# Optimization experiments

Measured on AMD Instinct MI355X. Metric: run time of the kernel, lower is better.

Reference implementation:

```python
import jax, jax.numpy as jnp
import numpy as np

B, LC, LA = 512, 128, 16
VOCAB, E, H, POL = 100000, 300, 300, 3


def _lstm_dir(x, W_ih, W_hh, b):
    # x: [B,T,E] -> h: [B,T,H]; PyTorch gate order i,f,g,o
    xg = jnp.einsum('bte,ge->btg', x, W_ih) + b  # [B,T,4H]
    h0 = jnp.zeros((x.shape[0], W_hh.shape[1]), x.dtype)

    def step(carry, xt):
        h, c = carry
        g = xt + h @ W_hh.T
        i, f, gg, o = jnp.split(g, 4, axis=-1)
        c = jax.nn.sigmoid(f) * c + jax.nn.sigmoid(i) * jnp.tanh(gg)
        h = jax.nn.sigmoid(o) * jnp.tanh(c)
        return (h, c), h

    _, hs = jax.lax.scan(step, (h0, h0), jnp.swapaxes(xg, 0, 1))
    return jnp.swapaxes(hs, 0, 1)


def _bilstm(x, lengths, Wif, Whf, bf, Wib, Whb, bb):
    # DynamicLSTM semantics: valid positions only, zero-padded outputs.
    T = x.shape[1]
    t = jnp.arange(T)
    mask = t[None, :] < lengths[:, None]
    h_f = _lstm_dir(x, Wif, Whf, bf)
    # reverse each sequence within its valid length for the backward direction
    ridx = jnp.where(mask, lengths[:, None] - 1 - t[None, :], t[None, :])
    x_rev = jnp.take_along_axis(x, ridx[:, :, None], axis=1)
    h_b = jnp.take_along_axis(_lstm_dir(x_rev, Wib, Whb, bb), ridx[:, :, None], axis=1)
    out = jnp.concatenate([h_f, h_b], axis=-1)
    return out * mask[:, :, None].astype(out.dtype)


def _mgan(text_raw, aspect, text_left, embed, cWif, cWhf, cbf, cWib, cWhb, cbb,
          aWif, aWhf, abf, aWib, aWhb, abb, w_u, w_a2c, w_c2a, dW, db):
    ctx_len = jnp.sum(text_raw != 0, axis=1)
    asp_len = jnp.sum(aspect != 0, axis=1)
    left_len = jnp.sum(text_left != 0, axis=1)
    start, end = left_len, left_len + asp_len - 1
    ctx = embed[text_raw]  # [B,LC,E]
    asp = embed[aspect]    # [B,LA,E]
    ctx_out = _bilstm(ctx, ctx_len, cWif, cWhf, cbf, cWib, cWhb, cbb)  # [B,LC,2H]
    asp_out = _bilstm(asp, asp_len, aWif, aWhf, abf, aWib, aWhb, abb)  # [B,LA,2H]
    # LocationEncoding (vectorized weight_matrix)
    T = text_raw.shape[1]
    j = jnp.arange(T)[None, :]
    sl = (T - asp_len)[:, None].astype(ctx_out.dtype)
    s, e = start[:, None], end[:, None]
    w = jnp.where(j < s, 1.0 - (s - j) / sl,
                  jnp.where(j <= e, 0.0, 1.0 - (j - e) / sl)).astype(ctx_out.dtype)
    ctx_out = ctx_out * w[:, :, None]
    ctx_pool = jnp.sum(ctx_out, axis=1) / ctx_len[:, None].astype(ctx_out.dtype)  # [B,2H]
    asp_pool = jnp.sum(asp_out, axis=1) / asp_len[:, None].astype(asp_out.dtype)  # [B,2H]
    # AlignmentMatrix as one batched bilinear: w_u = [w1; w2; w3]
    w1, w2, w3 = jnp.split(w_u[:, 0], 3)
    align = (ctx_out @ w1)[:, :, None] + (asp_out @ w2)[:, None, :] \
        + jnp.einsum('bid,bjd,d->bij', ctx_out, asp_out, w3)  # [B,LC,LA]
    f_asp2ctx = jnp.einsum('bid,bi->bd', ctx_out, jax.nn.softmax(align.max(axis=2), axis=1))
    f_ctx2asp = jnp.einsum('bjd,bj->bd', asp_out, jax.nn.softmax(align.max(axis=1), axis=1))
    a1 = jax.nn.softmax(jnp.einsum('bid,de,be->bi', ctx_out, w_a2c, asp_pool), axis=1)
    c_asp2ctx = jnp.einsum('bid,bi->bd', ctx_out, a1)
    a2 = jax.nn.softmax(jnp.einsum('bjd,de,be->bj', asp_out, w_c2a, ctx_pool), axis=1)
    c_ctx2asp = jnp.einsum('bjd,bj->bd', asp_out, a2)
    feat = jnp.concatenate([c_asp2ctx, f_asp2ctx, f_ctx2asp, c_ctx2asp], axis=1)  # [B,8H]
    return feat @ dW.T + db


def setup_inputs() -> dict:
    rng = np.random.RandomState(0)
    left = rng.randint(5, 61, size=B)
    alen = rng.randint(2, LA + 1, size=B)
    right = rng.randint(5, 46, size=B)
    clen = left + alen + right  # <= 121 <= LC
    text_raw = np.zeros((B, LC), np.int64)
    aspect = np.zeros((B, LA), np.int64)
    text_left = np.zeros((B, LC), np.int64)
    for i in range(B):
        text_raw[i, :clen[i]] = rng.randint(1, VOCAB, size=clen[i])
        aspect[i, :alen[i]] = rng.randint(1, VOCAB, size=alen[i])
        text_left[i, :left[i]] = rng.randint(1, VOCAB, size=left[i])
    ks = jax.random.split(jax.random.key(0), 18)
    kk = 1.0 / np.sqrt(H)
    u = lambda k_, sh: jax.random.uniform(k_, sh, jnp.float32, -kk, kk)
    return {
        'text_raw_indices': jnp.asarray(text_raw),
        'aspect_indices': jnp.asarray(aspect),
        'text_left_indices': jnp.asarray(text_left),
        'embed': jax.random.normal(ks[0], (VOCAB, E), jnp.float32) * 0.1,
        'cWif': u(ks[1], (4 * H, E)), 'cWhf': u(ks[2], (4 * H, H)), 'cbf': u(ks[3], (4 * H,)),
        'cWib': u(ks[4], (4 * H, E)), 'cWhb': u(ks[5], (4 * H, H)), 'cbb': u(ks[6], (4 * H,)),
        'aWif': u(ks[7], (4 * H, E)), 'aWhf': u(ks[8], (4 * H, H)), 'abf': u(ks[9], (4 * H,)),
        'aWib': u(ks[10], (4 * H, E)), 'aWhb': u(ks[11], (4 * H, H)), 'abb': u(ks[12], (4 * H,)),
        'w_u': jax.random.normal(ks[13], (6 * H, 1), jnp.float32) * 0.05,
        'w_a2c': jax.random.normal(ks[14], (2 * H, 2 * H), jnp.float32) * 0.05,
        'w_c2a': jax.random.normal(ks[15], (2 * H, 2 * H), jnp.float32) * 0.05,
        'dW': u(ks[16], (POL, 8 * H)), 'db': u(ks[17], (POL,)),
    }


def reference(text_raw_indices, aspect_indices, text_left_indices, embed,
              cWif, cWhf, cbf, cWib, cWhb, cbb,
              aWif, aWhf, abf, aWib, aWhb, abb,
              w_u, w_a2c, w_c2a, dW, db):
    return _mgan(text_raw_indices, aspect_indices, text_left_indices, embed,
                 cWif, cWhf, cbf, cWib, cWhb, cbb,
                 aWif, aWhf, abf, aWib, aWhb, abb,
                 w_u, w_a2c, w_c2a, dW, db)
```

## Files before the change

kernel.cpp:

```cpp
#include <hip/hip_runtime.h>
#include <math.h>

#define BB 512
#define LC 128
#define LA 16
#define EE 300
#define HH 300
#define D2 600

__device__ __forceinline__ float sigf(float x){ return 1.0f/(1.0f+expf(-x)); }

__global__ void k_lengths(const int* __restrict__ traw, const int* __restrict__ tasp,
                          const int* __restrict__ tleft,
                          int* __restrict__ clen, int* __restrict__ alen, int* __restrict__ sstart){
  int b = blockIdx.x*blockDim.x + threadIdx.x;
  if (b >= BB) return;
  int c=0,a=0,l=0;
  for (int t=0;t<LC;t++) c += (traw[b*LC+t]!=0);
  for (int t=0;t<LA;t++) a += (tasp[b*LA+t]!=0);
  for (int t=0;t<LC;t++) l += (tleft[b*LC+t]!=0);
  clen[b]=c; alen[b]=a; sstart[b]=l;
}

__global__ void k_prep(const float* __restrict__ cWif,const float* __restrict__ cWhf,
                       const float* __restrict__ cWib,const float* __restrict__ cWhb,
                       const float* __restrict__ aWif,const float* __restrict__ aWhf,
                       const float* __restrict__ aWib,const float* __restrict__ aWhb,
                       float* __restrict__ WT4){
  const int m = blockIdx.z;
  const float* src;
  switch(m){
    case 0: src=cWif; break; case 1: src=cWhf; break;
    case 2: src=cWib; break; case 3: src=cWhb; break;
    case 4: src=aWif; break; case 5: src=aWhf; break;
    case 6: src=aWib; break; default: src=aWhb; break;
  }
  int rem = blockIdx.x*blockDim.x + threadIdx.x;
  if (rem >= 90000) return;
  int kq = rem/1200, n = rem - kq*1200;
  float4 v = *(const float4*)(src + (size_t)n*300 + kq*4);
  ((float4*)WT4)[(size_t)m*90000 + rem] = v;
}

__device__ __forceinline__ void kloop8(const float (*__restrict__ src)[300],
                                       const float* __restrict__ W,
                                       float* a0, float* a1, float* a2,
                                       int n0, int n1, int n2, bool has3){
  const float4* Wp = (const float4*)W;
  for (int kq=0; kq<75; ++kq){
    float4 w0 = Wp[n0];
    float4 w1 = Wp[n1];
    #pragma unroll
    for (int r=0;r<8;r++){
      float4 h4 = *(const float4*)&src[r][4*kq];
      a0[r]=fmaf(w0.w,h4.w,fmaf(w0.z,h4.z,fmaf(w0.y,h4.y,fmaf(w0.x,h4.x,a0[r]))));
      a1[r]=fmaf(w1.w,h4.w,fmaf(w1.z,h4.z,fmaf(w1.y,h4.y,fmaf(w1.x,h4.x,a1[r]))));
    }
    if (has3){
      float4 w2 = Wp[n2];
      #pragma unroll
      for (int r=0;r<8;r++){
        float4 h4 = *(const float4*)&src[r][4*kq];
        a2[r]=fmaf(w2.w,h4.w,fmaf(w2.z,h4.z,fmaf(w2.y,h4.y,fmaf(w2.x,h4.x,a2[r]))));
      }
    }
    Wp += 1200;
  }
}

__launch_bounds__(512,1)
__global__ void k_xg(const int* __restrict__ traw, const float* __restrict__ embed,
                     const float* __restrict__ WT4,
                     const float* __restrict__ cbf, const float* __restrict__ cbb,
                     const int* __restrict__ clen,
                     float* __restrict__ xgcf, float* __restrict__ xgcb){
  const int bid = blockIdx.x;
  const int dir = bid & 1;
  const int blkInJob = bid >> 1;
  const float* Wi = WT4 + (size_t)(dir?2:0)*360000;
  const float* bias = dir ? cbb : cbf;
  float* xg = dir ? xgcb : xgcf;
  const int tid = threadIdx.x;
  const int n0=tid, n1=tid+512, n2=tid+1024;
  const bool has3 = tid<176;

  __shared__ __align__(16) float emb16[16][300];
  __shared__ int tk[16];

  const float b0 = bias[n0], b1 = bias[n1], b2 = has3 ? bias[n2] : 0.f;

  for (int tile = blkInJob; tile < 4096; tile += 256){
    const int b = tile >> 3;
    const int t0 = (tile & 7)*16;
    const int len = clen[b];
    if (t0 >= len) continue;
    const int cnt = min(16, len - t0);
    if (tid < 16){
      int t = t0 + tid;
      int pos = dir ? (len-1-t) : t;
      tk[tid] = (tid < cnt) ? traw[b*LC + pos] : 0;
    }
    __syncthreads();
    for (int idx=tid; idx<cnt*300; idx+=512){
      int r = idx/300, e = idx - r*300;
      emb16[r][e] = embed[(size_t)tk[r]*EE + e];
    }
    __syncthreads();

    float a0[16], a1[16], a2[16];
    #pragma unroll
    for (int r=0;r<16;r++){ a0[r]=b0; a1[r]=b1; a2[r]=b2; }
    {
      const float4* Wp = (const float4*)Wi;
      for (int kq=0; kq<75; ++kq){
        float4 w0 = Wp[n0];
        float4 w1 = Wp[n1];
        #pragma unroll
        for (int r=0;r<16;r++){
          float4 h4 = *(const float4*)&emb16[r][4*kq];
          a0[r]=fmaf(w0.w,h4.w,fmaf(w0.z,h4.z,fmaf(w0.y,h4.y,fmaf(w0.x,h4.x,a0[r]))));
          a1[r]=fmaf(w1.w,h4.w,fmaf(w1.z,h4.z,fmaf(w1.y,h4.y,fmaf(w1.x,h4.x,a1[r]))));
        }
        if (has3){
          float4 w2 = Wp[n2];
          #pragma unroll
          for (int r=0;r<16;r++){
            float4 h4 = *(const float4*)&emb16[r][4*kq];
            a2[r]=fmaf(w2.w,h4.w,fmaf(w2.z,h4.z,fmaf(w2.y,h4.y,fmaf(w2.x,h4.x,a2[r]))));
          }
        }
        Wp += 1200;
      }
    }
    #pragma unroll
    for (int r=0;r<16;r++){
      if (r < cnt){
        size_t base = ((size_t)b*LC + t0 + r)*1200;
        xg[base+n0]=a0[r]; xg[base+n1]=a1[r];
        if (has3) xg[base+n2]=a2[r];
      }
    }
    __syncthreads();
  }
}

__launch_bounds__(512,1)
__global__ void k_rec(const int* __restrict__ traw, const int* __restrict__ tasp,
                      const float* __restrict__ embed,
                      const float* __restrict__ WT4,
                      const float* __restrict__ cbf, const float* __restrict__ cbb,
                      const float* __restrict__ abf, const float* __restrict__ abb,
                      const float* __restrict__ xgcf, const float* __restrict__ xgcb,
                      const int* __restrict__ clen, const int* __restrict__ alen,
                      const int* __restrict__ sstart,
                      float* __restrict__ ctx_out, float* __restrict__ asp_out, int use_xg)
{
  const int tid = threadIdx.x;
  const int job = blockIdx.x & 3;
  const int sub = blockIdx.x >> 2;
  const int row0 = sub*8;
  const int isCtx = (job < 2), bwd = (job & 1);
  const int T = isCtx ? LC : LA;
  const int* lenp = isCtx ? clen : alen;
  const int* tokp = isCtx ? traw : tasp;
  const float* Wi = WT4 + (size_t)(job*2)*360000;
  const float* Wh = Wi + 360000;
  const float* bias = (job==0)?cbf:(job==1)?cbb:(job==2)?abf:abb;
  float* outb = isCtx ? ctx_out : asp_out;
  const int coloff = bwd ? 300 : 0;
  const int fuseX = isCtx ? (!use_xg) : 1;
  const float* xg = bwd ? xgcb : xgcf;

  __shared__ __align__(16) float hb[2][8][300];
  __shared__ __align__(16) float xb[8][300];
  __shared__ float gs[8][1200];
  __shared__ int  tok_s[8][LC];
  __shared__ int  len_s[8];
  __shared__ float wins[8], wine[8], winl[8];

  if (fuseX){
    for (int idx=tid; idx<8*T; idx+=512){ int r=idx/T, t=idx-r*T; tok_s[r][t]=tokp[(row0+r)*T+t]; }
  }
  if (tid < 8){
    int b = row0 + tid; len_s[tid] = lenp[b];
    if (isCtx){ float s=(float)sstart[b], a=(float)alen[b];
      wins[tid]=s; wine[tid]=s+a-1.0f; winl[tid]=(float)LC - a; }
  }
  for (int idx=tid; idx<2400; idx+=512){ int r=idx/300, d=idx-r*300; hb[0][r][d]=0.f; }
  __syncthreads();
  int maxl=0;
  #pragma unroll
  for (int r=0;r<8;r++) maxl = max(maxl, len_s[r]);

  const int n0=tid, n1=tid+512, n2=tid+1024;
  const bool has3 = tid<176;
  float b0=0.f,b1=0.f,b2=0.f;
  if (fuseX){ b0=bias[n0]; b1=bias[n1]; b2=has3?bias[n2]:0.f; }
  float creg[5];
  #pragma unroll
  for (int s=0;s<5;s++) creg[s]=0.f;
  int cur=0;

  for (int t=0; t<maxl; ++t){
    if (fuseX){
      for (int idx=tid; idx<2400; idx+=512){
        int r=idx/300, d=idx-r*300;
        int L=len_s[r];
        int ts = bwd ? ((t<L)?(L-1-t):t) : t;
        xb[r][d] = embed[(size_t)tok_s[r][ts]*EE + d];
      }
    }
    __syncthreads();

    float a0[8], a1[8], a2[8];
    if (fuseX){
      #pragma unroll
      for (int r=0;r<8;r++){ a0[r]=b0; a1[r]=b1; a2[r]=b2; }
      kloop8(xb, Wi, a0, a1, a2, n0, n1, n2, has3);
    } else {
      #pragma unroll
      for (int r=0;r<8;r++){
        int L=len_s[r];
        if (t < L){
          size_t base = ((size_t)(row0+r)*LC + t)*1200;
          a0[r]=xg[base+n0]; a1[r]=xg[base+n1]; a2[r]=has3?xg[base+n2]:0.f;
        } else { a0[r]=0.f; a1[r]=0.f; a2[r]=0.f; }
      }
    }
    kloop8(hb[cur], Wh, a0, a1, a2, n0, n1, n2, has3);

    #pragma unroll
    for (int r=0;r<8;r++){ gs[r][n0]=a0[r]; gs[r][n1]=a1[r]; if(has3) gs[r][n2]=a2[r]; }
    __syncthreads();

    #pragma unroll
    for (int s=0;s<5;s++){
      int idx = tid + s*512;
      if (idx < 2400){
        int r = idx/300, j = idx - r*300;
        int L = len_s[r];
        if (t < L){
          float gi=gs[r][j], gf=gs[r][300+j], gg=gs[r][600+j], go=gs[r][900+j];
          float cn = sigf(gf)*creg[s] + sigf(gi)*tanhf(gg);
          float hn = sigf(go)*tanhf(cn);
          creg[s]=cn;
          hb[cur^1][r][j]=hn;
          int tpos = bwd ? (L-1-t) : t;
          float wgt = 1.0f;
          if (isCtx){
            float jf=(float)tpos, s_=wins[r], e_=wine[r], sl=winl[r];
            wgt = (jf<s_)?(1.0f-(s_-jf)/sl):((jf<=e_)?0.0f:(1.0f-(jf-e_)/sl));
          }
          outb[((size_t)(row0+r)*T + tpos)*(size_t)D2 + coloff + j] = hn*wgt;
        }
      }
    }
    cur ^= 1;
  }
}

__global__ void k_pool(const float* __restrict__ ctx_out, const float* __restrict__ asp_out,
                       const int* __restrict__ clen, const int* __restrict__ alen,
                       float* __restrict__ ctx_pool, float* __restrict__ asp_pool){
  const int b=blockIdx.x; const int tid=threadIdx.x;
  for (int d=tid; d<D2; d+=blockDim.x){
    float s=0.f;
    for (int t=0;t<LC;t++) s+=ctx_out[((size_t)b*LC+t)*D2+d];
    ctx_pool[(size_t)b*D2+d]=s/(float)clen[b];
    float s2=0.f;
    for (int t=0;t<LA;t++) s2+=asp_out[((size_t)b*LA+t)*D2+d];
    asp_pool[(size_t)b*D2+d]=s2/(float)alen[b];
  }
}

__global__ void k_v1v2(const float* __restrict__ w_a2c, const float* __restrict__ w_c2a,
                       const float* __restrict__ ctx_pool, const float* __restrict__ asp_pool,
                       float* __restrict__ v1, float* __restrict__ v2){
  const int b=blockIdx.x; const int tid=threadIdx.x;
  __shared__ __align__(16) float ap[600];
  __shared__ __align__(16) float cp[600];
  for (int d=tid;d<600;d+=256){ ap[d]=asp_pool[(size_t)b*D2+d]; cp[d]=ctx_pool[(size_t)b*D2+d]; }
  __syncthreads();
  for (int d=tid;d<600;d+=256){
    const float4* ra=(const float4*)(w_a2c+(size_t)d*600);
    const float4* rc=(const float4*)(w_c2a+(size_t)d*600);
    float s1=0.f,s2=0.f;
    for (int e4=0;e4<150;e4++){
      float4 wa=ra[e4], wc=rc[e4];
      const float4 av=*(const float4*)&ap[4*e4];
      const float4 cv=*(const float4*)&cp[4*e4];
      s1 = fmaf(wa.w,av.w,fmaf(wa.z,av.z,fmaf(wa.y,av.y,fmaf(wa.x,av.x,s1))));
      s2 = fmaf(wc.w,cv.w,fmaf(wc.z,cv.z,fmaf(wc.y,cv.y,fmaf(wc.x,cv.x,s2))));
    }
    v1[(size_t)b*D2+d]=s1; v2[(size_t)b*D2+d]=s2;
  }
}

__launch_bounds__(256,2)
__global__ void k_attn(const float* __restrict__ ctx_out, const float* __restrict__ asp_out,
                       const float* __restrict__ v1, const float* __restrict__ v2,
                       const float* __restrict__ w_u, const float* __restrict__ dW,
                       const float* __restrict__ db, float* __restrict__ out)
{
  const int b = blockIdx.x;
  const int tid = threadIdx.x;
  const int wv = tid>>6, lane = tid&63;

  __shared__ float asp[16][600];
  __shared__ float w1s[600], w3s[600], v1s[600], v2s[600];
  __shared__ float u2s[16], m2w[4][16];
  __shared__ float m1s[128], s1s[128];
  __shared__ float alph[128], a1s[128];
  __shared__ float bet[16], a2s[16], m2f[16], s2s[16];
  __shared__ float red[256];
  __shared__ float feat[2400];

  for (int idx=tid; idx<16*600; idx+=256){
    int j=idx/600, d=idx-j*600;
    asp[j][d]=asp_out[((size_t)b*LA+j)*D2+d];
  }
  for (int d=tid; d<600; d+=256){
    w1s[d]=w_u[d]; w3s[d]=w_u[1200+d];
    v1s[d]=v1[(size_t)b*D2+d]; v2s[d]=v2[(size_t)b*D2+d];
  }
  if (tid<64) m2w[tid>>4][tid&15] = -1e30f;
  __syncthreads();
  if (tid<16){
    float s=0.f;
    for (int d=0;d<600;d++) s += asp[tid][d]*w_u[600+d];
    u2s[tid]=s;
  }
  __syncthreads();

  float m2p[16];
  #pragma unroll
  for (int j=0;j<16;j++) m2p[j]=-1e30f;

  for (int i=wv; i<LC; i+=4){
    const float* crow = ctx_out + ((size_t)b*LC+i)*D2;
    float u1p=0.f, s1p=0.f, accj[16];
    #pragma unroll
    for (int j=0;j<16;j++) accj[j]=0.f;
    for (int m=0;m<10;m++){
      int d = lane + m*64;
      if (d<600){
        float v = crow[d];
        u1p = fmaf(v,w1s[d],u1p);
        s1p = fmaf(v,v1s[d],s1p);
        float cw = v*w3s[d];
        #pragma unroll
        for (int j=0;j<16;j++) accj[j] = fmaf(cw,asp[j][d],accj[j]);
      }
    }
    #pragma unroll
    for (int off=32; off>0; off>>=1){
      u1p += __shfl_xor(u1p,off);
      s1p += __shfl_xor(s1p,off);
      #pragma unroll
      for (int j=0;j<16;j++) accj[j] += __shfl_xor(accj[j],off);
    }
    float mj=-1e30f;
    #pragma unroll
    for (int j=0;j<16;j++){
      float a = u2s[j]+accj[j];
      mj = fmaxf(mj,a);
      m2p[j] = fmaxf(m2p[j], u1p+accj[j]);
    }
    if (lane==0){ m1s[i]=u1p+mj; s1s[i]=s1p; }
  }
  if (lane<16) m2w[wv][lane]=m2p[lane];
  __syncthreads();

  {
    float x1 = (tid<128)? m1s[tid] : -1e30f;
    red[tid]=x1; __syncthreads();
    for (int s=128;s>0;s>>=1){ if (tid<s) red[tid]=fmaxf(red[tid],red[tid+s]); __syncthreads(); }
    float M1=red[0]; __syncthreads();
    float e1=(tid<128)?expf(x1-M1):0.f;
    red[tid]=e1; __syncthreads();
    for (int s=128;s>0;s>>=1){ if (tid<s) red[tid]+=red[tid+s]; __syncthreads(); }
    float S1=red[0]; __syncthreads();
    if (tid<128) alph[tid]=e1/S1;

    float x2 = (tid<128)? s1s[tid] : -1e30f;
    red[tid]=x2; __syncthreads();
    for (int s=128;s>0;s>>=1){ if (tid<s) red[tid]=fmaxf(red[tid],red[tid+s]); __syncthreads(); }
    float M2=red[0]; __syncthreads();
    float e2=(tid<128)?expf(x2-M2):0.f;
    red[tid]=e2; __syncthreads();
    for (int s=128;s>0;s>>=1){ if (tid<s) red[tid]+=red[tid+s]; __syncthreads(); }
    float S2=red[0]; __syncthreads();
    if (tid<128) a1s[tid]=e2/S2;
  }

  if (tid<16){
    float m=-1e30f;
    #pragma unroll
    for (int w=0;w<4;w++) m=fmaxf(m,m2w[w][tid]);
    m2f[tid]=u2s[tid]+m;
    float s=0.f;
    for (int d=0;d<600;d++) s = fmaf(asp[tid][d],v2s[d],s);
    s2s[tid]=s;
  }
  __syncthreads();
  if (tid==0){
    float M=-1e30f,S=0.f;
    for (int j=0;j<16;j++) M=fmaxf(M,m2f[j]);
    for (int j=0;j<16;j++){ float e=expf(m2f[j]-M); bet[j]=e; S+=e; }
    for (int j=0;j<16;j++) bet[j]/=S;
    M=-1e30f;S=0.f;
    for (int j=0;j<16;j++) M=fmaxf(M,s2s[j]);
    for (int j=0;j<16;j++){ float e=expf(s2s[j]-M); a2s[j]=e; S+=e; }
    for (int j=0;j<16;j++) a2s[j]/=S;
  }
  __syncthreads();

  {
    const bool has2 = (tid<88);
    float fa0=0,fa1=0,fa2=0, ca0=0,ca1=0,ca2=0;
    for (int i=0;i<LC;i++){
      float al=alph[i], aa=a1s[i];
      const float* crow = ctx_out + ((size_t)b*LC+i)*D2;
      float x0=crow[tid];      fa0=fmaf(al,x0,fa0); ca0=fmaf(aa,x0,ca0);
      float x1=crow[tid+256];  fa1=fmaf(al,x1,fa1); ca1=fmaf(aa,x1,ca1);
      if (has2){ float x2=crow[tid+512]; fa2=fmaf(al,x2,fa2); ca2=fmaf(aa,x2,ca2); }
    }
    feat[tid]=ca0;           feat[600+tid]=fa0;
    feat[tid+256]=ca1;       feat[600+tid+256]=fa1;
    if (has2){ feat[tid+512]=ca2; feat[600+tid+512]=fa2; }

    float fc0=0,fc1=0,fc2=0, cc0=0,cc1=0,cc2=0;
    for (int j=0;j<16;j++){
      float be=bet[j], a2=a2s[j];
      float x0=asp[j][tid];      fc0=fmaf(be,x0,fc0); cc0=fmaf(a2,x0,cc0);
      float x1=asp[j][tid+256];  fc1=fmaf(be,x1,fc1); cc1=fmaf(a2,x1,cc1);
      if (has2){ float x2=asp[j][tid+512]; fc2=fmaf(be,x2,fc2); cc2=fmaf(a2,x2,cc2); }
    }
    feat[1200+tid]=fc0;        feat[1800+tid]=cc0;
    feat[1200+tid+256]=fc1;    feat[1800+tid+256]=cc1;
    if (has2){ feat[1200+tid+512]=fc2; feat[1800+tid+512]=cc2; }
  }
  __syncthreads();

  {
    float p0=0,p1=0,p2=0;
    for (int e=tid;e<2400;e+=256){
      float f=feat[e];
      p0=fmaf(f,dW[e],p0); p1=fmaf(f,dW[2400+e],p1); p2=fmaf(f,dW[4800+e],p2);
    }
    red[tid]=p0; __syncthreads();
    for (int s=128;s>0;s>>=1){ if (tid<s) red[tid]+=red[tid+s]; __syncthreads(); }
    if (tid==0) out[b*3+0]=red[0]+db[0];
    __syncthreads();
    red[tid]=p1; __syncthreads();
    for (int s=128;s>0;s>>=1){ if (tid<s) red[tid]+=red[tid+s]; __syncthreads(); }
    if (tid==0) out[b*3+1]=red[0]+db[1];
    __syncthreads();
    red[tid]=p2; __syncthreads();
    for (int s=128;s>0;s>>=1){ if (tid<s) red[tid]+=red[tid+s]; __syncthreads(); }
    if (tid==0) out[b*3+2]=red[0]+db[2];
  }
}

extern "C" void kernel_launch(void* const* d_in, const int* in_sizes, int n_in,
                              void* d_out, int out_size, void* d_ws, size_t ws_size,
                              hipStream_t stream) {
  const int*   traw =(const int*)d_in[0];
  const int*   tasp =(const int*)d_in[1];
  const int*   tleft=(const int*)d_in[2];
  const float* embed=(const float*)d_in[3];
  const float* cWif=(const float*)d_in[4];
  const float* cWhf=(const float*)d_in[5];
  const float* cbf =(const float*)d_in[6];
  const float* cWib=(const float*)d_in[7];
  const float* cWhb=(const float*)d_in[8];
  const float* cbb =(const float*)d_in[9];
  const float* aWif=(const float*)d_in[10];
  const float* aWhf=(const float*)d_in[11];
  const float* abf =(const float*)d_in[12];
  const float* aWib=(const float*)d_in[13];
  const float* aWhb=(const float*)d_in[14];
  const float* abb =(const float*)d_in[15];
  const float* w_u =(const float*)d_in[16];
  const float* w_a2c=(const float*)d_in[17];
  const float* w_c2a=(const float*)d_in[18];
  const float* dW  =(const float*)d_in[19];
  const float* db  =(const float*)d_in[20];
  float* out = (float*)d_out;

  char* w = (char*)d_ws;
  size_t o = 0;
  float* ctx_out  = (float*)(w+o); o += (size_t)BB*LC*D2*4;
  float* asp_out  = (float*)(w+o); o += (size_t)BB*LA*D2*4;
  float* WT4      = (float*)(w+o); o += (size_t)8*360000*4;
  float* ctx_pool = (float*)(w+o); o += (size_t)BB*D2*4;
  float* asp_pool = (float*)(w+o); o += (size_t)BB*D2*4;
  float* v1       = (float*)(w+o); o += (size_t)BB*D2*4;
  float* v2       = (float*)(w+o); o += (size_t)BB*D2*4;
  int*   clen     = (int*)(w+o);   o += (size_t)BB*4;
  int*   alen_    = (int*)(w+o);   o += (size_t)BB*4;
  int*   sstart   = (int*)(w+o);   o += (size_t)BB*4;
  size_t xg_bytes = (size_t)BB*LC*1200*4;
  float* xgcf     = (float*)(w+o);
  float* xgcb     = (float*)(w+o+xg_bytes);
  const int use_xg = (ws_size >= o + 2*xg_bytes) ? 1 : 0;
  if (!use_xg){ xgcf = (float*)w; xgcb = (float*)w; }

  hipMemsetAsync(ctx_out, 0, (size_t)BB*LC*D2*4 + (size_t)BB*LA*D2*4, stream);

  k_lengths<<<4,128,0,stream>>>(traw,tasp,tleft,clen,alen_,sstart);
  k_prep<<<dim3(352,1,8),256,0,stream>>>(cWif,cWhf,cWib,cWhb,aWif,aWhf,aWib,aWhb,WT4);
  if (use_xg)
    k_xg<<<512,512,0,stream>>>(traw,embed,WT4,cbf,cbb,clen,xgcf,xgcb);

  k_rec<<<256,512,0,stream>>>(traw,tasp,embed,WT4,
                              cbf,cbb,abf,abb,
                              xgcf,xgcb,
                              clen,alen_,sstart,
                              ctx_out,asp_out,use_xg);

  k_pool<<<512,256,0,stream>>>(ctx_out,asp_out,clen,alen_,ctx_pool,asp_pool);
  k_v1v2<<<512,256,0,stream>>>(w_a2c,w_c2a,ctx_pool,asp_pool,v1,v2);
  k_attn<<<512,256,0,stream>>>(ctx_out,asp_out,v1,v2,w_u,dW,db,out);
}
```

Before: 7.436 ms.

## Move LSTM recurrence to bf16 MFMA with split-precision weights and chunked input projection

Replaces the FP32 FMA input-projection and recurrence kernels with a single MFMA kernel. Weights are pre-swizzled into bf16 hi/lo fragment pairs, so two MFMA passes approximate FP32 precision. The input projection is computed for four timesteps at a time, with the gates interleaved per hidden unit, and stored as bf16 in a per-block scratch buffer. Each block handles 16 sequences instead of 8, which halves the block count, and blocks are mapped to jobs with XCD awareness. The hidden state and embeddings are still rounded to bf16 (the hi/lo split applies only to the weights), and the input gates are stored in bf16, so this adds precision risk. An FP32 fallback path is kept for when the workspace is too small.

```diff
diff --git a/kernel.cpp b/kernel.cpp
--- a/kernel.cpp
+++ b/kernel.cpp
@@ -2,13 +2,24 @@
 #include <math.h>
 
 #define BB 512
-#define LC 128
-#define LA 16
-#define EE 300
-#define HH 300
+#define LCC 128
+#define LAA 16
 #define D2 600
+#define NT 80
+#define KT 10
+#define NP 1280
+#define TC 4
+
+typedef __attribute__((ext_vector_type(8))) short bf16x8;
+typedef __attribute__((ext_vector_type(4))) float f32x4;
 
 __device__ __forceinline__ float sigf(float x){ return 1.0f/(1.0f+expf(-x)); }
+__device__ __forceinline__ unsigned short f2bf(float f){
+  unsigned u = __float_as_uint(f);
+  unsigned r = (u + 0x7FFFu + ((u>>16)&1u)) >> 16;
+  return (unsigned short)r;
+}
+__device__ __forceinline__ float bf2f(unsigned short h){ return __uint_as_float(((unsigned)h)<<16); }
 
 __global__ void k_lengths(const int* __restrict__ traw, const int* __restrict__ tasp,
                           const int* __restrict__ tleft,
@@ -16,17 +27,230 @@
   int b = blockIdx.x*blockDim.x + threadIdx.x;
   if (b >= BB) return;
   int c=0,a=0,l=0;
-  for (int t=0;t<LC;t++) c += (traw[b*LC+t]!=0);
-  for (int t=0;t<LA;t++) a += (tasp[b*LA+t]!=0);
-  for (int t=0;t<LC;t++) l += (tleft[b*LC+t]!=0);
+  for (int t=0;t<LCC;t++) c += (traw[b*LCC+t]!=0);
+  for (int t=0;t<LAA;t++) a += (tasp[b*LAA+t]!=0);
+  for (int t=0;t<LCC;t++) l += (tleft[b*LCC+t]!=0);
   clen[b]=c; alen[b]=a; sstart[b]=l;
 }
 
-__global__ void k_prep(const float* __restrict__ cWif,const float* __restrict__ cWhf,
-                       const float* __restrict__ cWib,const float* __restrict__ cWhb,
-                       const float* __restrict__ aWif,const float* __restrict__ aWhf,
-                       const float* __restrict__ aWib,const float* __restrict__ aWhb,
-                       float* __restrict__ WT4){
+__global__ void k_prep_frag(const float* __restrict__ cWif,const float* __restrict__ cWhf,
+                            const float* __restrict__ cWib,const float* __restrict__ cWhb,
+                            const float* __restrict__ aWif,const float* __restrict__ aWhf,
+                            const float* __restrict__ aWib,const float* __restrict__ aWhb,
+                            short* __restrict__ Wfrag){
+  const int m = blockIdx.y;
+  const float* W;
+  switch(m){ case 0:W=cWif;break; case 1:W=cWhf;break; case 2:W=cWib;break; case 3:W=cWhb;break;
+             case 4:W=aWif;break; case 5:W=aWhf;break; case 6:W=aWib;break; default:W=aWhb;break; }
+  const int nt = blockIdx.x/KT, kt = blockIdx.x%KT;
+  const int lane = threadIdx.x;
+  const int np = nt*16 + (lane&15);
+  const int g  = lane>>4;
+  const int n  = (np<1200) ? 300*(np&3) + (np>>2) : -1;
+  size_t bi_hi = (((((size_t)m*2+0)*NT + nt)*KT + kt)*64 + lane)*8;
+  size_t bi_lo = (((((size_t)m*2+1)*NT + nt)*KT + kt)*64 + lane)*8;
+  #pragma unroll
+  for (int e=0;e<8;++e){
+    int k = kt*32 + 4*g + (e&3) + 16*(e>>2);
+    float v = (n>=0 && k<300) ? W[(size_t)n*300+k] : 0.f;
+    unsigned short hi = f2bf(v);
+    float lo = v - bf2f(hi);
+    Wfrag[bi_hi+e] = (short)hi;
+    Wfrag[bi_lo+e] = (short)f2bf(lo);
+  }
+}
+
+__global__ void k_prep_bias(const float* __restrict__ cbf,const float* __restrict__ cbb,
+                            const float* __restrict__ abf,const float* __restrict__ abb,
+                            float* __restrict__ bias_p){
+  int j = blockIdx.x;
+  int np = blockIdx.y*256 + threadIdx.x;
+  if (np>=NP) return;
+  const float* b = (j==0)?cbf:(j==1)?cbb:(j==2)?abf:abb;
+  bias_p[j*NP+np] = (np<1200) ? b[300*(np&3)+(np>>2)] : 0.f;
+}
+
+__launch_bounds__(512,1)
+__global__ void k_rec_mfma(const int* __restrict__ traw, const int* __restrict__ tasp,
+                           const float* __restrict__ embed,
+                           const short* __restrict__ Wfrag, const float* __restrict__ bias_p,
+                           const int* __restrict__ clen, const int* __restrict__ alen,
+                           const int* __restrict__ sstart,
+                           short* __restrict__ xg_all,
+                           float* __restrict__ ctx_out, float* __restrict__ asp_out)
+{
+  const int tid = threadIdx.x;
+  const int lane = tid & 63;
+  const int wv = tid >> 6;
+  const int bid = blockIdx.x;
+  const int xcd = bid & 7;
+  const int job = xcd >> 1;
+  const int wj  = (bid >> 3)*2 + (xcd & 1);
+  const int row0 = wj*16;
+  const int isCtx = (job<2), bwd = (job&1);
+  const int T = isCtx ? LCC : LAA;
+  const int* lenp = isCtx ? clen : alen;
+  const int* tokp = isCtx ? traw : tasp;
+  float* outb = isCtx ? ctx_out : asp_out;
+  const int coloff = bwd ? 300 : 0;
+  const short* WiF = Wfrag + (size_t)(job*2+0)*819200;
+  const short* WhF = Wfrag + (size_t)(job*2+1)*819200;
+  short* xg = xg_all + (size_t)bid * (16*TC*NP);
+
+  __shared__ short hfrag[KT][64][8];
+  __shared__ float gs[16][1284];
+  __shared__ int   tok_s[16][LCC];
+  __shared__ float biasL[NP];
+  __shared__ int   len_s[16];
+  __shared__ float wins[16], wine[16], winl[16];
+  short* stg = (short*)&gs[0][0];
+
+  for (int i=tid; i<16*T; i+=512){ int r=i/T, t=i-r*T; tok_s[r][t]=tokp[(row0+r)*T+t]; }
+  if (tid<16){
+    int b=row0+tid; len_s[tid]=lenp[b];
+    if (isCtx){ float s=(float)sstart[b], a=(float)alen[b];
+      wins[tid]=s; wine[tid]=s+a-1.0f; winl[tid]=(float)LCC - a; }
+  }
+  for (int i=tid;i<NP;i+=512) biasL[i]=bias_p[job*NP+i];
+  for (int i=tid;i<KT*64*8;i+=512) ((short*)hfrag)[i]=0;
+  float cst[10];
+  #pragma unroll
+  for (int s=0;s<10;++s) cst[s]=0.f;
+  __syncthreads();
+  int maxl=0;
+  #pragma unroll
+  for (int r=0;r<16;++r) maxl = max(maxl, len_s[r]);
+
+  const int nt0 = wv*10;
+  const int col = lane & 15, lg = lane >> 4;
+
+  for (int t0=0; t0<maxl; t0+=TC){
+    {
+      const int tc = wv & 3, kth = wv >> 2;
+      const int t = t0 + tc;
+      const int r = col;
+      const int L = len_s[r];
+      int pos = bwd ? (L-1-t) : t;
+      if (t >= L) pos = 0;
+      const float* erow = embed + (size_t)tok_s[r][pos]*300;
+      for (int kt=kth*5; kt<kth*5+5; ++kt){
+        const int k0 = kt*32 + 4*lg;
+        float4 pa = {0.f,0.f,0.f,0.f}, pb = {0.f,0.f,0.f,0.f};
+        if (k0+3  < 300) pa = *(const float4*)(erow + k0);
+        if (k0+19 < 300) pb = *(const float4*)(erow + k0 + 16);
+        bf16x8 pk;
+        pk[0]=(short)f2bf(pa.x); pk[1]=(short)f2bf(pa.y); pk[2]=(short)f2bf(pa.z); pk[3]=(short)f2bf(pa.w);
+        pk[4]=(short)f2bf(pb.x); pk[5]=(short)f2bf(pb.y); pk[6]=(short)f2bf(pb.z); pk[7]=(short)f2bf(pb.w);
+        ((bf16x8*)stg)[(tc*KT + kt)*64 + lane] = pk;
+      }
+    }
+    __syncthreads();
+    {
+      f32x4 acc[4][10];
+      #pragma unroll
+      for (int m=0;m<4;++m){
+        #pragma unroll
+        for (int i=0;i<10;++i) acc[m][i] = (f32x4){0.f,0.f,0.f,0.f};
+      }
+      #pragma unroll
+      for (int pass=0; pass<2; ++pass){
+        const bf16x8* B = (const bf16x8*)(WiF + (size_t)pass*409600);
+        for (int kt=0; kt<KT; ++kt){
+          bf16x8 a0 = ((const bf16x8*)stg)[(0*KT+kt)*64 + lane];
+          bf16x8 a1 = ((const bf16x8*)stg)[(1*KT+kt)*64 + lane];
+          bf16x8 a2 = ((const bf16x8*)stg)[(2*KT+kt)*64 + lane];
+          bf16x8 a3 = ((const bf16x8*)stg)[(3*KT+kt)*64 + lane];
+          #pragma unroll
+          for (int ntl=0; ntl<10; ++ntl){
+            bf16x8 bb = B[(size_t)((nt0+ntl)*KT + kt)*64 + lane];
+            acc[0][ntl] = __builtin_amdgcn_mfma_f32_16x16x32_bf16(a0, bb, acc[0][ntl], 0,0,0);
+            acc[1][ntl] = __builtin_amdgcn_mfma_f32_16x16x32_bf16(a1, bb, acc[1][ntl], 0,0,0);
+            acc[2][ntl] = __builtin_amdgcn_mfma_f32_16x16x32_bf16(a2, bb, acc[2][ntl], 0,0,0);
+            acc[3][ntl] = __builtin_amdgcn_mfma_f32_16x16x32_bf16(a3, bb, acc[3][ntl], 0,0,0);
+          }
+        }
+      }
+      #pragma unroll
+      for (int ntl=0; ntl<10; ++ntl){
+        int np = (nt0+ntl)*16 + col;
+        float bv = biasL[np];
+        #pragma unroll
+        for (int m=0;m<4;++m){
+          #pragma unroll
+          for (int q=0;q<4;++q){
+            int r = lg*4 + q;
+            xg[((size_t)r*TC + m)*NP + np] = (short)f2bf(acc[m][ntl][q] + bv);
+          }
+        }
+      }
+    }
+    __syncthreads();
+    const int tend = min(TC, maxl - t0);
+    for (int tc=0; tc<tend; ++tc){
+      const int t = t0 + tc;
+      f32x4 ga[10];
+      #pragma unroll
+      for (int i=0;i<10;++i) ga[i] = (f32x4){0.f,0.f,0.f,0.f};
+      #pragma unroll
+      for (int pass=0; pass<2; ++pass){
+        const bf16x8* B = (const bf16x8*)(WhF + (size_t)pass*409600);
+        for (int kt=0; kt<KT; ++kt){
+          bf16x8 a = *(const bf16x8*)&hfrag[kt][lane][0];
+          #pragma unroll
+          for (int ntl=0; ntl<10; ++ntl){
+            bf16x8 bb = B[(size_t)((nt0+ntl)*KT + kt)*64 + lane];
+            ga[ntl] = __builtin_amdgcn_mfma_f32_16x16x32_bf16(a, bb, ga[ntl], 0,0,0);
+          }
+        }
+      }
+      #pragma unroll
+      for (int ntl=0; ntl<10; ++ntl){
+        int np = (nt0+ntl)*16 + col;
+        #pragma unroll
+        for (int q=0;q<4;++q) gs[lg*4+q][np] = ga[ntl][q];
+      }
+      __syncthreads();
+      #pragma unroll
+      for (int s=0;s<10;++s){
+        int idx = tid + s*512;
+        if (idx < 4800){
+          int r = idx/300, j = idx - r*300;
+          int L = len_s[r];
+          if (t < L){
+            float4 gq = *(const float4*)&gs[r][4*j];
+            unsigned long long raw = __hip_atomic_load(
+              (const unsigned long long*)(xg + ((size_t)r*TC + tc)*NP + 4*j),
+              __ATOMIC_RELAXED, __HIP_MEMORY_SCOPE_AGENT);
+            float gi = gq.x + bf2f((unsigned short)( raw        & 0xFFFF));
+            float gf = gq.y + bf2f((unsigned short)((raw >> 16) & 0xFFFF));
+            float gg2= gq.z + bf2f((unsigned short)((raw >> 32) & 0xFFFF));
+            float go = gq.w + bf2f((unsigned short)((raw >> 48) & 0xFFFF));
+            float cn = sigf(gf)*cst[s] + sigf(gi)*tanhf(gg2);
+            float hn = sigf(go)*tanhf(cn);
+            cst[s] = cn;
+            int kt2 = j>>5, kk = j&31;
+            int g2 = (kk&15)>>2, e = (kk&3) + 4*(kk>>4);
+            hfrag[kt2][g2*16 + r][e] = (short)f2bf(hn);
+            int tpos = bwd ? (L-1-t) : t;
+            float wgt = 1.0f;
+            if (isCtx){
+              float jf=(float)tpos, s_=wins[r], e_=wine[r], sl=winl[r];
+              wgt = (jf<s_)?(1.0f-(s_-jf)/sl):((jf<=e_)?0.0f:(1.0f-(jf-e_)/sl));
+            }
+            outb[((size_t)(row0+r)*T + tpos)*(size_t)D2 + coloff + j] = hn*wgt;
+          }
+        }
+      }
+      __syncthreads();
+    }
+  }
+}
+
+__global__ void k_prep_f32(const float* __restrict__ cWif,const float* __restrict__ cWhf,
+                           const float* __restrict__ cWib,const float* __restrict__ cWhb,
+                           const float* __restrict__ aWif,const float* __restrict__ aWhf,
+                           const float* __restrict__ aWib,const float* __restrict__ aWhb,
+                           float* __restrict__ WT4){
   const int m = blockIdx.z;
   const float* src;
   switch(m){
@@ -69,98 +293,21 @@
 }
 
 __launch_bounds__(512,1)
-__global__ void k_xg(const int* __restrict__ traw, const float* __restrict__ embed,
-                     const float* __restrict__ WT4,
-                     const float* __restrict__ cbf, const float* __restrict__ cbb,
-                     const int* __restrict__ clen,
-                     float* __restrict__ xgcf, float* __restrict__ xgcb){
-  const int bid = blockIdx.x;
-  const int dir = bid & 1;
-  const int blkInJob = bid >> 1;
-  const float* Wi = WT4 + (size_t)(dir?2:0)*360000;
-  const float* bias = dir ? cbb : cbf;
-  float* xg = dir ? xgcb : xgcf;
-  const int tid = threadIdx.x;
-  const int n0=tid, n1=tid+512, n2=tid+1024;
-  const bool has3 = tid<176;
-
-  __shared__ __align__(16) float emb16[16][300];
-  __shared__ int tk[16];
-
-  const float b0 = bias[n0], b1 = bias[n1], b2 = has3 ? bias[n2] : 0.f;
-
-  for (int tile = blkInJob; tile < 4096; tile += 256){
-    const int b = tile >> 3;
-    const int t0 = (tile & 7)*16;
-    const int len = clen[b];
-    if (t0 >= len) continue;
-    const int cnt = min(16, len - t0);
-    if (tid < 16){
-      int t = t0 + tid;
-      int pos = dir ? (len-1-t) : t;
-      tk[tid] = (tid < cnt) ? traw[b*LC + pos] : 0;
-    }
-    __syncthreads();
-    for (int idx=tid; idx<cnt*300; idx+=512){
-      int r = idx/300, e = idx - r*300;
-      emb16[r][e] = embed[(size_t)tk[r]*EE + e];
-    }
-    __syncthreads();
-
-    float a0[16], a1[16], a2[16];
-    #pragma unroll
-    for (int r=0;r<16;r++){ a0[r]=b0; a1[r]=b1; a2[r]=b2; }
-    {
-      const float4* Wp = (const float4*)Wi;
-      for (int kq=0; kq<75; ++kq){
-        float4 w0 = Wp[n0];
-        float4 w1 = Wp[n1];
-        #pragma unroll
-        for (int r=0;r<16;r++){
-          float4 h4 = *(const float4*)&emb16[r][4*kq];
-          a0[r]=fmaf(w0.w,h4.w,fmaf(w0.z,h4.z,fmaf(w0.y,h4.y,fmaf(w0.x,h4.x,a0[r]))));
-          a1[r]=fmaf(w1.w,h4.w,fmaf(w1.z,h4.z,fmaf(w1.y,h4.y,fmaf(w1.x,h4.x,a1[r]))));
-        }
-        if (has3){
-          float4 w2 = Wp[n2];
-          #pragma unroll
-          for (int r=0;r<16;r++){
-            float4 h4 = *(const float4*)&emb16[r][4*kq];
-            a2[r]=fmaf(w2.w,h4.w,fmaf(w2.z,h4.z,fmaf(w2.y,h4.y,fmaf(w2.x,h4.x,a2[r]))));
-          }
-        }
-        Wp += 1200;
-      }
-    }
-    #pragma unroll
-    for (int r=0;r<16;r++){
-      if (r < cnt){
-        size_t base = ((size_t)b*LC + t0 + r)*1200;
-        xg[base+n0]=a0[r]; xg[base+n1]=a1[r];
-        if (has3) xg[base+n2]=a2[r];
-      }
-    }
-    __syncthreads();
-  }
-}
-
-__launch_bounds__(512,1)
-__global__ void k_rec(const int* __restrict__ traw, const int* __restrict__ tasp,
-                      const float* __restrict__ embed,
-                      const float* __restrict__ WT4,
-                      const float* __restrict__ cbf, const float* __restrict__ cbb,
-                      const float* __restrict__ abf, const float* __restrict__ abb,
-                      const float* __restrict__ xgcf, const float* __restrict__ xgcb,
-                      const int* __restrict__ clen, const int* __restrict__ alen,
-                      const int* __restrict__ sstart,
-                      float* __restrict__ ctx_out, float* __restrict__ asp_out, int use_xg)
+__global__ void k_rec_f32(const int* __restrict__ traw, const int* __restrict__ tasp,
+                          const float* __restrict__ embed,
+                          const float* __restrict__ WT4,
+                          const float* __restrict__ cbf, const float* __restrict__ cbb,
+                          const float* __restrict__ abf, const float* __restrict__ abb,
+                          const int* __restrict__ clen, const int* __restrict__ alen,
+                          const int* __restrict__ sstart,
+                          float* __restrict__ ctx_out, float* __restrict__ asp_out)
 {
   const int tid = threadIdx.x;
   const int job = blockIdx.x & 3;
   const int sub = blockIdx.x >> 2;
   const int row0 = sub*8;
   const int isCtx = (job < 2), bwd = (job & 1);
-  const int T = isCtx ? LC : LA;
+  const int T = isCtx ? LCC : LAA;
   const int* lenp = isCtx ? clen : alen;
   const int* tokp = isCtx ? traw : tasp;
   const float* Wi = WT4 + (size_t)(job*2)*360000;
@@ -168,69 +315,51 @@
   const float* bias = (job==0)?cbf:(job==1)?cbb:(job==2)?abf:abb;
   float* outb = isCtx ? ctx_out : asp_out;
   const int coloff = bwd ? 300 : 0;
-  const int fuseX = isCtx ? (!use_xg) : 1;
-  const float* xg = bwd ? xgcb : xgcf;
 
   __shared__ __align__(16) float hb[2][8][300];
   __shared__ __align__(16) float xb[8][300];
-  __shared__ float gs[8][1200];
-  __shared__ int  tok_s[8][LC];
-  __shared__ int  len_s[8];
-  __shared__ float wins[8], wine[8], winl[8];
-
-  if (fuseX){
-    for (int idx=tid; idx<8*T; idx+=512){ int r=idx/T, t=idx-r*T; tok_s[r][t]=tokp[(row0+r)*T+t]; }
-  }
+  __shared__ float gsf[8][1200];
+  __shared__ int  tok_s2[8][LCC];
+  __shared__ int  len_s2[8];
+  __shared__ float wins2[8], wine2[8], winl2[8];
+
+  for (int idx=tid; idx<8*T; idx+=512){ int r=idx/T, t=idx-r*T; tok_s2[r][t]=tokp[(row0+r)*T+t]; }
   if (tid < 8){
-    int b = row0 + tid; len_s[tid] = lenp[b];
+    int b = row0 + tid; len_s2[tid] = lenp[b];
     if (isCtx){ float s=(float)sstart[b], a=(float)alen[b];
-      wins[tid]=s; wine[tid]=s+a-1.0f; winl[tid]=(float)LC - a; }
+      wins2[tid]=s; wine2[tid]=s+a-1.0f; winl2[tid]=(float)LCC - a; }
   }
   for (int idx=tid; idx<2400; idx+=512){ int r=idx/300, d=idx-r*300; hb[0][r][d]=0.f; }
   __syncthreads();
   int maxl=0;
   #pragma unroll
-  for (int r=0;r<8;r++) maxl = max(maxl, len_s[r]);
+  for (int r=0;r<8;r++) maxl = max(maxl, len_s2[r]);
 
   const int n0=tid, n1=tid+512, n2=tid+1024;
   const bool has3 = tid<176;
-  float b0=0.f,b1=0.f,b2=0.f;
-  if (fuseX){ b0=bias[n0]; b1=bias[n1]; b2=has3?bias[n2]:0.f; }
+  float b0=bias[n0], b1=bias[n1], b2=has3?bias[n2]:0.f;
   float creg[5];
   #pragma unroll
   for (int s=0;s<5;s++) creg[s]=0.f;
   int cur=0;
 
   for (int t=0; t<maxl; ++t){
-    if (fuseX){
-      for (int idx=tid; idx<2400; idx+=512){
-        int r=idx/300, d=idx-r*300;
-        int L=len_s[r];
-        int ts = bwd ? ((t<L)?(L-1-t):t) : t;
-        xb[r][d] = embed[(size_t)tok_s[r][ts]*EE + d];
-      }
+    for (int idx=tid; idx<2400; idx+=512){
+      int r=idx/300, d=idx-r*300;
+      int L=len_s2[r];
+      int ts = bwd ? ((t<L)?(L-1-t):t) : t;
+      xb[r][d] = embed[(size_t)tok_s2[r][ts]*300 + d];
     }
     __syncthreads();
 
     float a0[8], a1[8], a2[8];
-    if (fuseX){
-      #pragma unroll
-      for (int r=0;r<8;r++){ a0[r]=b0; a1[r]=b1; a2[r]=b2; }
-      kloop8(xb, Wi, a0, a1, a2, n0, n1, n2, has3);
-    } else {
-      #pragma unroll
-      for (int r=0;r<8;r++){
-        int L=len_s[r];
-        if (t < L){
-          size_t base = ((size_t)(row0+r)*LC + t)*1200;
-          a0[r]=xg[base+n0]; a1[r]=xg[base+n1]; a2[r]=has3?xg[base+n2]:0.f;
-        } else { a0[r]=0.f; a1[r]=0.f; a2[r]=0.f; }
-      }
-    }
+    #pragma unroll
+    for (int r=0;r<8;r++){ a0[r]=b0; a1[r]=b1; a2[r]=b2; }
+    kloop8(xb, Wi, a0, a1, a2, n0, n1, n2, has3);
     kloop8(hb[cur], Wh, a0, a1, a2, n0, n1, n2, has3);
 
     #pragma unroll
-    for (int r=0;r<8;r++){ gs[r][n0]=a0[r]; gs[r][n1]=a1[r]; if(has3) gs[r][n2]=a2[r]; }
+    for (int r=0;r<8;r++){ gsf[r][n0]=a0[r]; gsf[r][n1]=a1[r]; if(has3) gsf[r][n2]=a2[r]; }
     __syncthreads();
 
     #pragma unroll
@@ -238,9 +367,9 @@
       int idx = tid + s*512;
       if (idx < 2400){
         int r = idx/300, j = idx - r*300;
-        int L = len_s[r];
+        int L = len_s2[r];
         if (t < L){
-          float gi=gs[r][j], gf=gs[r][300+j], gg=gs[r][600+j], go=gs[r][900+j];
+          float gi=gsf[r][j], gf=gsf[r][300+j], gg=gsf[r][600+j], go=gsf[r][900+j];
           float cn = sigf(gf)*creg[s] + sigf(gi)*tanhf(gg);
           float hn = sigf(go)*tanhf(cn);
           creg[s]=cn;
@@ -248,7 +377,7 @@
           int tpos = bwd ? (L-1-t) : t;
           float wgt = 1.0f;
           if (isCtx){
-            float jf=(float)tpos, s_=wins[r], e_=wine[r], sl=winl[r];
+            float jf=(float)tpos, s_=wins2[r], e_=wine2[r], sl=winl2[r];
             wgt = (jf<s_)?(1.0f-(s_-jf)/sl):((jf<=e_)?0.0f:(1.0f-(jf-e_)/sl));
           }
           outb[((size_t)(row0+r)*T + tpos)*(size_t)D2 + coloff + j] = hn*wgt;
@@ -265,10 +394,10 @@
   const int b=blockIdx.x; const int tid=threadIdx.x;
   for (int d=tid; d<D2; d+=blockDim.x){
     float s=0.f;
-    for (int t=0;t<LC;t++) s+=ctx_out[((size_t)b*LC+t)*D2+d];
+    for (int t=0;t<LCC;t++) s+=ctx_out[((size_t)b*LCC+t)*D2+d];
     ctx_pool[(size_t)b*D2+d]=s/(float)clen[b];
     float s2=0.f;
-    for (int t=0;t<LA;t++) s2+=asp_out[((size_t)b*LA+t)*D2+d];
+    for (int t=0;t<LAA;t++) s2+=asp_out[((size_t)b*LAA+t)*D2+d];
     asp_pool[(size_t)b*D2+d]=s2/(float)alen[b];
   }
 }
@@ -317,7 +446,7 @@
 
   for (int idx=tid; idx<16*600; idx+=256){
     int j=idx/600, d=idx-j*600;
-    asp[j][d]=asp_out[((size_t)b*LA+j)*D2+d];
+    asp[j][d]=asp_out[((size_t)b*LAA+j)*D2+d];
   }
   for (int d=tid; d<600; d+=256){
     w1s[d]=w_u[d]; w3s[d]=w_u[1200+d];
@@ -336,8 +465,8 @@
   #pragma unroll
   for (int j=0;j<16;j++) m2p[j]=-1e30f;
 
-  for (int i=wv; i<LC; i+=4){
-    const float* crow = ctx_out + ((size_t)b*LC+i)*D2;
+  for (int i=wv; i<LCC; i+=4){
+    const float* crow = ctx_out + ((size_t)b*LCC+i)*D2;
     float u1p=0.f, s1p=0.f, accj[16];
     #pragma unroll
     for (int j=0;j<16;j++) accj[j]=0.f;
@@ -418,9 +547,9 @@
   {
     const bool has2 = (tid<88);
     float fa0=0,fa1=0,fa2=0, ca0=0,ca1=0,ca2=0;
-    for (int i=0;i<LC;i++){
+    for (int i=0;i<LCC;i++){
       float al=alph[i], aa=a1s[i];
-      const float* crow = ctx_out + ((size_t)b*LC+i)*D2;
+      const float* crow = ctx_out + ((size_t)b*LCC+i)*D2;
       float x0=crow[tid];      fa0=fmaf(al,x0,fa0); ca0=fmaf(aa,x0,ca0);
       float x1=crow[tid+256];  fa1=fmaf(al,x1,fa1); ca1=fmaf(aa,x1,ca1);
       if (has2){ float x2=crow[tid+512]; fa2=fmaf(al,x2,fa2); ca2=fmaf(aa,x2,ca2); }
@@ -490,9 +619,9 @@
 
   char* w = (char*)d_ws;
   size_t o = 0;
-  float* ctx_out  = (float*)(w+o); o += (size_t)BB*LC*D2*4;
-  float* asp_out  = (float*)(w+o); o += (size_t)BB*LA*D2*4;
-  float* WT4      = (float*)(w+o); o += (size_t)8*360000*4;
+  float* ctx_out  = (float*)(w+o); o += (size_t)BB*LCC*D2*4;
+  float* asp_out  = (float*)(w+o); o += (size_t)BB*LAA*D2*4;
+  char*  Wshare   = (char*)(w+o);  o += (size_t)13107200;
   float* ctx_pool = (float*)(w+o); o += (size_t)BB*D2*4;
   float* asp_pool = (float*)(w+o); o += (size_t)BB*D2*4;
   float* v1       = (float*)(w+o); o += (size_t)BB*D2*4;
@@ -500,24 +629,26 @@
   int*   clen     = (int*)(w+o);   o += (size_t)BB*4;
   int*   alen_    = (int*)(w+o);   o += (size_t)BB*4;
   int*   sstart   = (int*)(w+o);   o += (size_t)BB*4;
-  size_t xg_bytes = (size_t)BB*LC*1200*4;
-  float* xgcf     = (float*)(w+o);
-  float* xgcb     = (float*)(w+o+xg_bytes);
-  const int use_xg = (ws_size >= o + 2*xg_bytes) ? 1 : 0;
-  if (!use_xg){ xgcf = (float*)w; xgcb = (float*)w; }
-
-  hipMemsetAsync(ctx_out, 0, (size_t)BB*LC*D2*4 + (size_t)BB*LA*D2*4, stream);
+  size_t need_base = o;
+  float* bias_p   = (float*)(w+o); o += (size_t)4*NP*4;
+  short* xg_all   = (short*)(w+o); o += (size_t)128*16*TC*NP*2;
+  const int use_mfma = (ws_size >= o) ? 1 : 0;
+  (void)need_base;
+
+  hipMemsetAsync(ctx_out, 0, (size_t)BB*LCC*D2*4 + (size_t)BB*LAA*D2*4, stream);
 
   k_lengths<<<4,128,0,stream>>>(traw,tasp,tleft,clen,alen_,sstart);
-  k_prep<<<dim3(352,1,8),256,0,stream>>>(cWif,cWhf,cWib,cWhb,aWif,aWhf,aWib,aWhb,WT4);
-  if (use_xg)
-    k_xg<<<512,512,0,stream>>>(traw,embed,WT4,cbf,cbb,clen,xgcf,xgcb);
-
-  k_rec<<<256,512,0,stream>>>(traw,tasp,embed,WT4,
-                              cbf,cbb,abf,abb,
-                              xgcf,xgcb,
-                              clen,alen_,sstart,
-                              ctx_out,asp_out,use_xg);
+
+  if (use_mfma){
+    k_prep_frag<<<dim3(NT*KT,8),64,0,stream>>>(cWif,cWhf,cWib,cWhb,aWif,aWhf,aWib,aWhb,(short*)Wshare);
+    k_prep_bias<<<dim3(4,5),256,0,stream>>>(cbf,cbb,abf,abb,bias_p);
+    k_rec_mfma<<<128,512,0,stream>>>(traw,tasp,embed,(const short*)Wshare,bias_p,
+                                     clen,alen_,sstart,xg_all,ctx_out,asp_out);
+  } else {
+    k_prep_f32<<<dim3(352,1,8),256,0,stream>>>(cWif,cWhf,cWib,cWhb,aWif,aWhf,aWib,aWhb,(float*)Wshare);
+    k_rec_f32<<<256,512,0,stream>>>(traw,tasp,embed,(const float*)Wshare,
+                                    cbf,cbb,abf,abb,clen,alen_,sstart,ctx_out,asp_out);
+  }
 
   k_pool<<<512,256,0,stream>>>(ctx_out,asp_out,clen,alen_,ctx_pool,asp_pool);
   k_v1v2<<<512,256,0,stream>>>(w_a2c,w_c2a,ctx_pool,asp_pool,v1,v2);
```

After: 13.71 ms. +84.4%, slower.
